# Optimization experiments

Measured on AMD Instinct MI355X. Metric: run time of the kernel, lower is better.

The kernel has to match this reference:

```python
import jax, jax.numpy as jnp
import numpy as np

FEAT_DIM = 128
GUIDE_DIM = 128
NIR_DIM = 32
H_LR, W_LR = 128, 128
H_HR, W_HR = 256, 256
IMNET_IN = FEAT_DIM + 2 * GUIDE_DIM + 2  # 386


def make_coord_1d(n):
    # pixel-center coords in [-1, 1]: (2i+1)/n - 1
    return (2.0 * jnp.arange(n, dtype=jnp.float32) + 1.0) / n - 1.0


def nearest_sample(img, cy, cx):
    """F.grid_sample(img, grid, mode='nearest', align_corners=False, padding='zeros').
    img: [b, C, h, w]; cy, cx: [N] normalized coords (cy -> h axis, cx -> w axis).
    Returns sampled values [b, C, N] and the pixel-center coords (qcy, qcx) the
    nearest sample corresponds to (0 when out of range, matching zero padding)."""
    h, w = img.shape[-2], img.shape[-1]
    iy = jnp.round(((cy + 1.0) * h - 1.0) * 0.5).astype(jnp.int32)  # round-half-even == nearbyint
    ix = jnp.round(((cx + 1.0) * w - 1.0) * 0.5).astype(jnp.int32)
    valid = (iy >= 0) & (iy < h) & (ix >= 0) & (ix < w)
    iyc = jnp.clip(iy, 0, h - 1)
    ixc = jnp.clip(ix, 0, w - 1)
    out = img[:, :, iyc, ixc]                       # [b, C, N] gather
    out = jnp.where(valid[None, None, :], out, 0.0)
    qcy = jnp.where(valid, (2.0 * iyc.astype(jnp.float32) + 1.0) / h - 1.0, 0.0)
    qcx = jnp.where(valid, (2.0 * ixc.astype(jnp.float32) + 1.0) / w - 1.0, 0.0)
    return out, qcy, qcx


def mlp(x, W1, b1, W2, b2, W3, b3):
    x = jax.nn.relu(x @ W1 + b1)
    x = jax.nn.relu(x @ W2 + b2)
    return x @ W3 + b3


def setup_inputs() -> dict:
    key = jax.random.key(0)
    ks = jax.random.split(key, 9)
    return {
        "feat": jax.random.normal(ks[0], (1, FEAT_DIM, H_LR, W_LR), jnp.float32),
        "lr_guide": jax.random.normal(ks[1], (1, GUIDE_DIM, H_LR, W_LR), jnp.float32),
        "hr_guide": jax.random.normal(ks[2], (1, GUIDE_DIM, H_HR, W_HR), jnp.float32),
        "W1": jax.random.normal(ks[3], (IMNET_IN, 256), jnp.float32) * 0.05,
        "b1": jax.random.normal(ks[4], (256,), jnp.float32) * 0.05,
        "W2": jax.random.normal(ks[5], (256, 128), jnp.float32) * 0.05,
        "b2": jax.random.normal(ks[6], (128,), jnp.float32) * 0.05,
        "W3": jax.random.normal(ks[7], (128, NIR_DIM), jnp.float32) * 0.05,
        "b3": jax.random.normal(ks[8], (NIR_DIM,), jnp.float32) * 0.05,
    }


def reference(feat, lr_guide, hr_guide, W1, b1, W2, b2, W3, b3):
    b, _, h, w = feat.shape
    _, cg, H, W = hr_guide.shape
    N = H * W
    featc = jnp.concatenate([lr_guide, feat], axis=1)        # [b, guide+feat, h, w]

    gy, gx = jnp.meshgrid(make_coord_1d(H), make_coord_1d(W), indexing="ij")
    cy = gy.reshape(-1)                                      # [N] coord[:, 0] (h axis)
    cx = gx.reshape(-1)                                      # [N] coord[:, 1] (w axis)

    q_guide_hr = hr_guide.reshape(b, cg, N).transpose(0, 2, 1)  # [b, N, cg]

    # feat_ : gather at the unshifted coord (identical across neighbors)
    feat_b, _, _ = nearest_sample(featc, cy, cx)
    feat_b = feat_b.transpose(0, 2, 1)                       # [b, N, C]

    rx = 1.0 / h
    ry = 1.0 / w
    preds, gcs = [], []
    for vx in (-1.0, 1.0):
        for vy in (-1.0, 1.0):
            q_feat, qcy, qcx = nearest_sample(featc, cy + vx * rx, cx + vy * ry)
            q_feat = q_feat.transpose(0, 2, 1)               # [b, N, C]
            rel = jnp.stack([(cy - qcy) * h, (cx - qcx) * w], axis=-1)  # [N, 2]
            rel = jnp.broadcast_to(rel[None], (b, N, 2))
            inp = jnp.concatenate([q_feat, q_guide_hr, rel], axis=-1)  # [b, N, 386]
            preds.append(mlp(inp, W1, b1, W2, b2, W3, b3))   # [b, N, NIR]
            # bilateral color weight: dot over channels [-4:-1]
            gcs.append(jnp.sum(feat_b[..., -4:-1] * q_feat[..., -4:-1], axis=-1))
    preds = jnp.stack(preds, axis=-1)                        # [b, N, NIR, 4]
    weight = jax.nn.softmax(jnp.stack(gcs, axis=-1), axis=-1)  # [b, N, 4]
    ret = jnp.sum(preds * weight[:, :, None, :], axis=-1)    # [b, N, NIR]
    return ret.transpose(0, 2, 1).reshape(b, -1, H, W)
```

## Files before the change

kernel.cpp:

```cpp
#include <hip/hip_runtime.h>
#include <hip/hip_bf16.h>


using bf16x8 = __attribute__((ext_vector_type(8))) __bf16;
using f32x4  = __attribute__((ext_vector_type(4))) float;

__device__ __forceinline__ float bf2f(unsigned short u){
  unsigned int x = ((unsigned int)u) << 16;
  return __builtin_bit_cast(float, x);
}
__device__ __forceinline__ unsigned short f2bf(float f){
  unsigned int x = __builtin_bit_cast(unsigned int, f);
  unsigned int r = x + 0x7fffu + ((x >> 16) & 1u);
  return (unsigned short)(r >> 16);
}
__device__ __forceinline__ unsigned int cvt_pk_bf16(float lo, float hi){
  unsigned int r;
  asm("v_cvt_pk_bf16_f32 %0, %1, %2" : "=v"(r) : "v"(lo), "v"(hi));
  return r;
}
__device__ __forceinline__ bf16x8 ld8(const ushort* p){
  uint4 r = *(const uint4*)p;
  return __builtin_bit_cast(bf16x8, r);
}

__device__ __forceinline__ int swzA(int row, int col){
  int p = ((row << 1) + (row >> 2)) & 7;
  return row*256 + (col ^ (p << 3));
}
__device__ __forceinline__ int swzB(int row, int col){
  int p = ((row << 1) + (row >> 2)) & 7;
  return row*128 + (col ^ (p << 3));
}
__device__ __forceinline__ int swzT(int row, int c){
  return row*256 + ((c & ~0x38) | ((((c>>3) + (c>>6) + row) & 7) << 3));
}

struct RowMeta { int spos; float relY, relX; };
__device__ __forceinline__ RowMeta row_meta(int Y, int X, int br){
  int ivx = br >> 1, ivy = br & 1;
  int validY, iy; float relY;
  if (ivx == 0){ validY = (Y >= 1);   iy = (Y-1) >> 1; relY = (Y & 1) ?  0.5f :  1.5f; }
  else         { validY = (Y <= 254); iy = (Y+1) >> 1; relY = (Y & 1) ? -1.5f : -0.5f; }
  int validX, ix; float relX;
  if (ivy == 0){ validX = (X >= 1);   ix = (X-1) >> 1; relX = (X & 1) ?  0.5f :  1.5f; }
  else         { validX = (X <= 254); ix = (X+1) >> 1; relX = (X & 1) ? -1.5f : -0.5f; }
  RowMeta r;
  if (validY && validX){ r.spos = iy*128 + ix; r.relY = relY; r.relX = relX; }
  else { r.spos = -1; r.relY = (float)Y + 0.5f - 128.0f; r.relX = (float)X + 0.5f - 128.0f; }
  return r;
}

__global__ __launch_bounds__(256) void prep(
    const float* __restrict__ W1, const float* __restrict__ W2,
    const float* __restrict__ W3,
    const float* __restrict__ lr_guide, const float* __restrict__ feat,
    ushort* __restrict__ W1t,
    ushort* __restrict__ W2t,
    ushort* __restrict__ W3t,
    ushort* __restrict__ Ft)
{
  __shared__ ushort T[32*256];
  const int b = blockIdx.x, t = threadIdx.x;
  if (b < 512){
    const int pos0 = b*32;
    #pragma unroll
    for (int i=0;i<32;i++){
      int k = i*8 + (t>>5), pos = t & 31;
      const float* src = (k < 128) ? lr_guide : feat;
      T[swzT(pos, k)] = f2bf(src[(size_t)(k & 127)*16384 + pos0 + pos]);
    }
    __syncthreads();
    const int pos = t>>3, ul = t&7;
    #pragma unroll
    for (int jj=0;jj<4;jj++){
      int c = ul*32 + jj*8;
      union { uint4 v; ushort s[8]; } x;
      x.v = *(const uint4*)&T[swzT(pos, c)];
      *(uint4*)&Ft[(size_t)(pos0+pos)*256 + c] = x.v;
    }
  } else {
    int i = (b-512)*256 + t;
    { int k = i >> 8, n = i & 255; W1t[n*384 + k] = f2bf(W1[i]); }
    if (i < 32768){ int k = i >> 7, n = i & 127; W2t[n*256 + k] = f2bf(W2[i]); }
    if (i < 4096) { int k = i >> 5, n = i & 31;  W3t[n*128 + k] = f2bf(W3[i]); }
  }
}

__global__ __launch_bounds__(256) void u_gemm(
    const ushort* __restrict__ Ft, const ushort* __restrict__ W1t,
    ushort* __restrict__ U)
{
  const int t = threadIdx.x;
  const int w = t >> 6, lane = t & 63, quad = lane >> 4, l15 = lane & 15;
  const int pos0 = (blockIdx.x >> 1) * 32;
  const int nh   = blockIdx.x & 1;

  bf16x8 af0[8], af1[8];
  #pragma unroll
  for (int kt=0; kt<8; kt++){
    const int ko = kt*32 + quad*8;
    af0[kt] = ld8(&Ft[(size_t)(pos0 +      l15)*256 + ko]);
    af1[kt] = ld8(&Ft[(size_t)(pos0 + 16 + l15)*256 + ko]);
  }
  f32x4 acc[2][2];
  #pragma unroll
  for (int a=0;a<2;a++){ acc[a][0] = f32x4{0.f,0.f,0.f,0.f}; acc[a][1] = f32x4{0.f,0.f,0.f,0.f}; }

  #pragma unroll
  for (int kt=0; kt<8; kt++){
    const int ko = kt*32 + quad*8;
    bf16x8 b0 = ld8(&W1t[(size_t)(nh*128 + w*32 +      l15)*384 + ko]);
    bf16x8 b1 = ld8(&W1t[(size_t)(nh*128 + w*32 + 16 + l15)*384 + ko]);
    acc[0][0] = __builtin_amdgcn_mfma_f32_16x16x32_bf16(af0[kt], b0, acc[0][0], 0,0,0);
    acc[0][1] = __builtin_amdgcn_mfma_f32_16x16x32_bf16(af0[kt], b1, acc[0][1], 0,0,0);
    acc[1][0] = __builtin_amdgcn_mfma_f32_16x16x32_bf16(af1[kt], b0, acc[1][0], 0,0,0);
    acc[1][1] = __builtin_amdgcn_mfma_f32_16x16x32_bf16(af1[kt], b1, acc[1][1], 0,0,0);
  }
  #pragma unroll
  for (int mt=0; mt<2; mt++)
    #pragma unroll
    for (int nt=0; nt<2; nt++){
      int n = nh*128 + w*32 + nt*16 + l15;
      #pragma unroll
      for (int r=0; r<4; r++)
        U[(size_t)(pos0 + mt*16 + quad*4 + r)*256 + n] = f2bf(acc[mt][nt][r]);
    }
}

__global__ __launch_bounds__(256, 4) void main_fused(
    const float* __restrict__ feat,
    const float* __restrict__ hr_guide,
    const float* __restrict__ W1,
    const float* __restrict__ b1v,
    const float* __restrict__ b2v,
    const float* __restrict__ b3v,
    const ushort* __restrict__ U,
    const ushort* __restrict__ W1t,
    const ushort* __restrict__ W2t,
    const ushort* __restrict__ W3t,
    float* __restrict__ outp)
{
  __shared__ __align__(16) ushort A1[64*256];
  __shared__ __align__(16) float  w1r[2][256];
  __shared__ float gcs[64];
  __shared__ float wgt[64];

  const int t = threadIdx.x;
  const int w = t >> 6, lane = t & 63, quad = lane >> 4, l15 = lane & 15;
  const int Y  = blockIdx.x >> 4;
  const int X0 = (blockIdx.x & 15) << 4;

  const int m   = t >> 2;
  const int cg  = t & 3;
  const int pix = m >> 2, br = m & 3;
  RowMeta rm = row_meta(Y, X0 + pix, br);

  uint4 uu[8];
  if (rm.spos >= 0){
    const ushort* Up = U + (size_t)rm.spos*256 + cg*8;
    #pragma unroll
    for (int jj=0; jj<8; jj++) uu[jj] = *(const uint4*)(Up + jj*32);
  } else {
    #pragma unroll
    for (int jj=0; jj<8; jj++) uu[jj] = make_uint4(0u,0u,0u,0u);
  }

  w1r[0][t] = W1[384*256 + t];
  w1r[1][t] = W1[385*256 + t];

  if (t < 64){
    RowMeta g = row_meta(Y, X0 + (t>>2), t & 3);
    float gc = 0.0f;
    if (g.spos >= 0){
      int bpos = (Y>>1)*128 + ((X0 + (t>>2)) >> 1);
      #pragma unroll
      for (int cc=0; cc<3; cc++)
        gc += feat[(size_t)(124+cc)*16384 + bpos] * feat[(size_t)(124+cc)*16384 + g.spos];
    }
    gcs[t] = gc;
  }

  {
    const float* hg = hr_guide + (size_t)Y*256 + X0 + l15;
    bf16x8 ha[4];
    #pragma unroll
    for (int kt=0; kt<4; kt++){
      float v[8];
      #pragma unroll
      for (int j=0; j<8; j++) v[j] = hg[(size_t)(kt*32 + quad*8 + j)*65536];
      uint4 pk;
      pk.x = cvt_pk_bf16(v[0],v[1]); pk.y = cvt_pk_bf16(v[2],v[3]);
      pk.z = cvt_pk_bf16(v[4],v[5]); pk.w = cvt_pk_bf16(v[6],v[7]);
      ha[kt] = __builtin_bit_cast(bf16x8, pk);
    }
    f32x4 accg[4];
    #pragma unroll
    for (int nt=0; nt<4; nt++) accg[nt] = f32x4{0.f,0.f,0.f,0.f};
    #pragma unroll
    for (int kt=0; kt<4; kt++)
      #pragma unroll
      for (int nt=0; nt<4; nt++){
        bf16x8 b = ld8(&W1t[(size_t)(w*64 + nt*16 + l15)*384 + 256 + kt*32 + quad*8]);
        accg[nt] = __builtin_amdgcn_mfma_f32_16x16x32_bf16(ha[kt], b, accg[nt], 0,0,0);
      }
    #pragma unroll
    for (int nt=0; nt<4; nt++){
      int n = w*64 + nt*16 + l15;
      float bv = b1v[n];
      #pragma unroll
      for (int r=0; r<4; r++)
        A1[swzA(32 + quad*4 + r, n)] = f2bf(accg[nt][r] + bv);
    }
  }
  __syncthreads();

  uint4 gt[8];
  #pragma unroll
  for (int jj=0; jj<8; jj++)
    gt[jj] = *(const uint4*)&A1[swzA(32 + pix, cg*8 + jj*32)];
  if (t < 16){
    float g0 = gcs[t*4+0], g1 = gcs[t*4+1], g2 = gcs[t*4+2], g3 = gcs[t*4+3];
    float mx = fmaxf(fmaxf(g0,g1), fmaxf(g2,g3));
    float e0 = __expf(g0-mx), e1 = __expf(g1-mx), e2 = __expf(g2-mx), e3 = __expf(g3-mx);
    float inv = 1.0f/(e0+e1+e2+e3);
    wgt[t*4+0]=e0*inv; wgt[t*4+1]=e1*inv; wgt[t*4+2]=e2*inv; wgt[t*4+3]=e3*inv;
  }
  __syncthreads();

  {
    const float relY = rm.relY, relX = rm.relX;
    #pragma unroll
    for (int jj=0; jj<8; jj++){
      const int c = cg*8 + jj*32;
      union { uint4 v; ushort s[8]; } gu, uv;
      gu.v = gt[jj];
      uv.v = uu[jj];
      float r0[8], r1[8];
      *(float4*)&r0[0] = *(const float4*)&w1r[0][c];
      *(float4*)&r0[4] = *(const float4*)&w1r[0][c+4];
      *(float4*)&r1[0] = *(const float4*)&w1r[1][c];
      *(float4*)&r1[4] = *(const float4*)&w1r[1][c+4];
      unsigned int ov[4];
      #pragma unroll
      for (int i=0; i<4; i++){
        float h0 = bf2f(uv.s[2*i+0]) + bf2f(gu.s[2*i+0]) + relY*r0[2*i+0] + relX*r1[2*i+0];
        float h1 = bf2f(uv.s[2*i+1]) + bf2f(gu.s[2*i+1]) + relY*r0[2*i+1] + relX*r1[2*i+1];
        ov[i] = cvt_pk_bf16(fmaxf(h0, 0.0f), fmaxf(h1, 0.0f));
      }
      *(uint4*)&A1[swzA(m, c)] = make_uint4(ov[0],ov[1],ov[2],ov[3]);
    }
  }
  __syncthreads();

  bf16x8 b2f[8][2];
  #pragma unroll
  for (int kt=0; kt<8; kt++)
    #pragma unroll
    for (int nt=0; nt<2; nt++)
      b2f[kt][nt] = ld8(&W2t[(size_t)(w*32 + nt*16 + l15)*256 + kt*32 + quad*8]);

  f32x4 acc2[4][2];
  #pragma unroll
  for (int mt=0; mt<4; mt++)
    #pragma unroll
    for (int nt=0; nt<2; nt++) acc2[mt][nt] = f32x4{0.f,0.f,0.f,0.f};

  __builtin_amdgcn_s_setprio(1);
  #pragma unroll
  for (int mt=0; mt<4; mt++)
    #pragma unroll
    for (int kt=0; kt<8; kt++){
      bf16x8 a = ld8(&A1[swzA(mt*16 + l15, kt*32 + quad*8)]);
      #pragma unroll
      for (int nt=0; nt<2; nt++)
        acc2[mt][nt] = __builtin_amdgcn_mfma_f32_16x16x32_bf16(a, b2f[kt][nt], acc2[mt][nt], 0,0,0);
    }
  __builtin_amdgcn_s_setprio(0);
  __syncthreads();

  bf16x8 b3f[4][2];
  #pragma unroll
  for (int kt=0; kt<4; kt++)
    #pragma unroll
    for (int nt=0; nt<2; nt++)
      b3f[kt][nt] = ld8(&W3t[(size_t)(nt*16 + l15)*128 + kt*32 + quad*8]);
  {
    float bias0 = b2v[w*32 + l15], bias1 = b2v[w*32 + 16 + l15];
    #pragma unroll
    for (int mt=0; mt<4; mt++)
      #pragma unroll
      for (int nt=0; nt<2; nt++){
        int n = w*32 + nt*16 + l15;
        float bv = nt ? bias1 : bias0;
        #pragma unroll
        for (int r=0; r<4; r++)
          A1[swzB(mt*16 + quad*4 + r, n)] = f2bf(fmaxf(acc2[mt][nt][r] + bv, 0.0f));
      }
  }
  __syncthreads();

  {
    f32x4 acc3[2] = { f32x4{0.f,0.f,0.f,0.f}, f32x4{0.f,0.f,0.f,0.f} };
    #pragma unroll
    for (int kt=0; kt<4; kt++){
      bf16x8 a = ld8(&A1[swzB(w*16 + l15, kt*32 + quad*8)]);
      #pragma unroll
      for (int nt=0; nt<2; nt++)
        acc3[nt] = __builtin_amdgcn_mfma_f32_16x16x32_bf16(a, b3f[kt][nt], acc3[nt], 0,0,0);
    }
    int lp = w*4 + quad;
    int X = X0 + lp;
    float w0 = wgt[lp*4+0], w1 = wgt[lp*4+1], w2 = wgt[lp*4+2], w3 = wgt[lp*4+3];
    #pragma unroll
    for (int nt=0; nt<2; nt++){
      int n = nt*16 + l15;
      float bb = b3v[n];
      float v = w0*(acc3[nt][0]+bb) + w1*(acc3[nt][1]+bb)
              + w2*(acc3[nt][2]+bb) + w3*(acc3[nt][3]+bb);
      outp[(size_t)n*65536 + (size_t)Y*256 + X] = v;
    }
  }
}

extern "C" void kernel_launch(void* const* d_in, const int* in_sizes, int n_in,
                              void* d_out, int out_size, void* d_ws, size_t ws_size,
                              hipStream_t stream)
{
  const float* feat     = (const float*)d_in[0];
  const float* lr_guide = (const float*)d_in[1];
  const float* hr_guide = (const float*)d_in[2];
  const float* W1       = (const float*)d_in[3];
  const float* b1       = (const float*)d_in[4];
  const float* W2       = (const float*)d_in[5];
  const float* b2       = (const float*)d_in[6];
  const float* W3       = (const float*)d_in[7];
  const float* b3       = (const float*)d_in[8];
  float* outp = (float*)d_out;

  char* ws = (char*)d_ws;
  ushort* W1t = (ushort*)(ws);
  ushort* W2t = (ushort*)(ws + 196608);
  ushort* W3t = (ushort*)(ws + 262144);
  ushort* Ft  = (ushort*)(ws + 270336);
  ushort* Ub  = (ushort*)(ws + 270336 + 8388608);

  prep<<<896, 256, 0, stream>>>(W1, W2, W3, lr_guide, feat, W1t, W2t, W3t, Ft);
  u_gemm<<<1024, 256, 0, stream>>>(Ft, W1t, Ub);
  main_fused<<<4096, 256, 0, stream>>>(feat, hr_guide, W1, b1, b2, b3,
                                       Ub, W1t, W2t, W3t, outp);
}
```

Baseline: 223.7 us.

## Fuse feature transpose into U GEMM and stage hr_guide via LDS

Drops the intermediate Ft buffer by having u_gemm transpose and convert lr_guide/feat tiles into shared memory itself, with each block computing all 256 output columns. In main_fused, hr_guide is loaded with coalesced float4 reads into LDS instead of strided scalar loads. The guide GEMM results go to a separate Gt buffer, W2 fragment loads are hoisted earlier, and a block-index swizzle is added. The extra LDS use and hoisted registers lower the occupancy hint from 4 to 3 blocks.

```diff
diff --git a/kernel.cpp b/kernel.cpp
--- a/kernel.cpp
+++ b/kernel.cpp
@@ -31,9 +31,6 @@
 __device__ __forceinline__ int swzB(int row, int col){
   int p = ((row << 1) + (row >> 2)) & 7;
   return row*128 + (col ^ (p << 3));
-}
-__device__ __forceinline__ int swzT(int row, int c){
-  return row*256 + ((c & ~0x38) | ((((c>>3) + (c>>6) + row) & 7) << 3));
 }
 
 struct RowMeta { int spos; float relY, relX; };
@@ -51,84 +48,70 @@
   return r;
 }
 
-__global__ __launch_bounds__(256) void prep(
+__global__ __launch_bounds__(256) void convert_weights(
     const float* __restrict__ W1, const float* __restrict__ W2,
     const float* __restrict__ W3,
-    const float* __restrict__ lr_guide, const float* __restrict__ feat,
     ushort* __restrict__ W1t,
     ushort* __restrict__ W2t,
-    ushort* __restrict__ W3t,
-    ushort* __restrict__ Ft)
+    ushort* __restrict__ W3t)
+{
+  int i = blockIdx.x*256 + threadIdx.x;
+  { int k = i >> 8, n = i & 255; W1t[n*384 + k] = f2bf(W1[i]); }
+  if (i < 32768){ int k = i >> 7, n = i & 127; W2t[n*256 + k] = f2bf(W2[i]); }
+  if (i < 4096) { int k = i >> 5, n = i & 31;  W3t[n*128 + k] = f2bf(W3[i]); }
+}
+
+__global__ __launch_bounds__(256) void u_gemm(
+    const float* __restrict__ lr_guide, const float* __restrict__ feat,
+    const ushort* __restrict__ W1t,
+    ushort* __restrict__ U)
 {
   __shared__ ushort T[32*256];
-  const int b = blockIdx.x, t = threadIdx.x;
-  if (b < 512){
-    const int pos0 = b*32;
-    #pragma unroll
-    for (int i=0;i<32;i++){
-      int k = i*8 + (t>>5), pos = t & 31;
-      const float* src = (k < 128) ? lr_guide : feat;
-      T[swzT(pos, k)] = f2bf(src[(size_t)(k & 127)*16384 + pos0 + pos]);
-    }
-    __syncthreads();
-    const int pos = t>>3, ul = t&7;
-    #pragma unroll
-    for (int jj=0;jj<4;jj++){
-      int c = ul*32 + jj*8;
-      union { uint4 v; ushort s[8]; } x;
-      x.v = *(const uint4*)&T[swzT(pos, c)];
-      *(uint4*)&Ft[(size_t)(pos0+pos)*256 + c] = x.v;
-    }
-  } else {
-    int i = (b-512)*256 + t;
-    { int k = i >> 8, n = i & 255; W1t[n*384 + k] = f2bf(W1[i]); }
-    if (i < 32768){ int k = i >> 7, n = i & 127; W2t[n*256 + k] = f2bf(W2[i]); }
-    if (i < 4096) { int k = i >> 5, n = i & 31;  W3t[n*128 + k] = f2bf(W3[i]); }
-  }
-}
-
-__global__ __launch_bounds__(256) void u_gemm(
-    const ushort* __restrict__ Ft, const ushort* __restrict__ W1t,
-    ushort* __restrict__ U)
-{
   const int t = threadIdx.x;
   const int w = t >> 6, lane = t & 63, quad = lane >> 4, l15 = lane & 15;
-  const int pos0 = (blockIdx.x >> 1) * 32;
-  const int nh   = blockIdx.x & 1;
-
-  bf16x8 af0[8], af1[8];
+  const int pos0 = blockIdx.x * 32;
+
+  #pragma unroll
+  for (int i=0; i<32; i++){
+    int k = i*8 + (t>>5), p = t & 31;
+    const float* src = (k < 128) ? lr_guide : feat;
+    T[swzA(p, k)] = f2bf(src[(size_t)(k & 127)*16384 + pos0 + p]);
+  }
+  __syncthreads();
+
+  f32x4 acc[2][4];
+  #pragma unroll
+  for (int mt=0; mt<2; mt++)
+    #pragma unroll
+    for (int nt=0; nt<4; nt++) acc[mt][nt] = f32x4{0.f,0.f,0.f,0.f};
+
   #pragma unroll
   for (int kt=0; kt<8; kt++){
     const int ko = kt*32 + quad*8;
-    af0[kt] = ld8(&Ft[(size_t)(pos0 +      l15)*256 + ko]);
-    af1[kt] = ld8(&Ft[(size_t)(pos0 + 16 + l15)*256 + ko]);
-  }
-  f32x4 acc[2][2];
-  #pragma unroll
-  for (int a=0;a<2;a++){ acc[a][0] = f32x4{0.f,0.f,0.f,0.f}; acc[a][1] = f32x4{0.f,0.f,0.f,0.f}; }
-
-  #pragma unroll
-  for (int kt=0; kt<8; kt++){
-    const int ko = kt*32 + quad*8;
-    bf16x8 b0 = ld8(&W1t[(size_t)(nh*128 + w*32 +      l15)*384 + ko]);
-    bf16x8 b1 = ld8(&W1t[(size_t)(nh*128 + w*32 + 16 + l15)*384 + ko]);
-    acc[0][0] = __builtin_amdgcn_mfma_f32_16x16x32_bf16(af0[kt], b0, acc[0][0], 0,0,0);
-    acc[0][1] = __builtin_amdgcn_mfma_f32_16x16x32_bf16(af0[kt], b1, acc[0][1], 0,0,0);
-    acc[1][0] = __builtin_amdgcn_mfma_f32_16x16x32_bf16(af1[kt], b0, acc[1][0], 0,0,0);
-    acc[1][1] = __builtin_amdgcn_mfma_f32_16x16x32_bf16(af1[kt], b1, acc[1][1], 0,0,0);
+    bf16x8 bt[4];
+    #pragma unroll
+    for (int nt=0; nt<4; nt++)
+      bt[nt] = ld8(&W1t[(size_t)(w*64 + nt*16 + l15)*384 + ko]);
+    bf16x8 a0 = ld8(&T[swzA(l15,      ko)]);
+    bf16x8 a1 = ld8(&T[swzA(16 + l15, ko)]);
+    #pragma unroll
+    for (int nt=0; nt<4; nt++){
+      acc[0][nt] = __builtin_amdgcn_mfma_f32_16x16x32_bf16(a0, bt[nt], acc[0][nt], 0,0,0);
+      acc[1][nt] = __builtin_amdgcn_mfma_f32_16x16x32_bf16(a1, bt[nt], acc[1][nt], 0,0,0);
+    }
   }
   #pragma unroll
   for (int mt=0; mt<2; mt++)
     #pragma unroll
-    for (int nt=0; nt<2; nt++){
-      int n = nh*128 + w*32 + nt*16 + l15;
+    for (int nt=0; nt<4; nt++){
+      int n = w*64 + nt*16 + l15;
       #pragma unroll
       for (int r=0; r<4; r++)
         U[(size_t)(pos0 + mt*16 + quad*4 + r)*256 + n] = f2bf(acc[mt][nt][r]);
     }
 }
 
-__global__ __launch_bounds__(256, 4) void main_fused(
+__global__ __launch_bounds__(256, 3) void main_fused(
     const float* __restrict__ feat,
     const float* __restrict__ hr_guide,
     const float* __restrict__ W1,
@@ -142,14 +125,16 @@
     float* __restrict__ outp)
 {
   __shared__ __align__(16) ushort A1[64*256];
+  __shared__ __align__(16) ushort Gt[16*256];
   __shared__ __align__(16) float  w1r[2][256];
   __shared__ float gcs[64];
   __shared__ float wgt[64];
 
   const int t = threadIdx.x;
   const int w = t >> 6, lane = t & 63, quad = lane >> 4, l15 = lane & 15;
-  const int Y  = blockIdx.x >> 4;
-  const int X0 = (blockIdx.x & 15) << 4;
+  const int wg = (blockIdx.x & 7) * 512 + (blockIdx.x >> 3);
+  const int Y  = wg >> 4;
+  const int X0 = (wg & 15) << 4;
 
   const int m   = t >> 2;
   const int cg  = t & 3;
@@ -166,6 +151,25 @@
     for (int jj=0; jj<8; jj++) uu[jj] = make_uint4(0u,0u,0u,0u);
   }
 
+  bf16x8 gb[4][4];
+  #pragma unroll
+  for (int kt=0; kt<4; kt++)
+    #pragma unroll
+    for (int nt=0; nt<4; nt++)
+      gb[kt][nt] = ld8(&W1t[(size_t)(w*64 + nt*16 + l15)*384 + 256 + kt*32 + quad*8]);
+
+  {
+    #pragma unroll
+    for (int i=0; i<2; i++){
+      int id = i*256 + t;
+      int ch = id >> 2, xq = id & 3;
+      float4 v = *(const float4*)(hr_guide + (size_t)ch*65536 + Y*256 + X0 + xq*4);
+      A1[swzB(xq*4+0, ch)] = f2bf(v.x);
+      A1[swzB(xq*4+1, ch)] = f2bf(v.y);
+      A1[swzB(xq*4+2, ch)] = f2bf(v.z);
+      A1[swzB(xq*4+3, ch)] = f2bf(v.w);
+    }
+  }
   w1r[0][t] = W1[384*256 + t];
   w1r[1][t] = W1[385*256 + t];
 
@@ -180,45 +184,8 @@
     }
     gcs[t] = gc;
   }
-
-  {
-    const float* hg = hr_guide + (size_t)Y*256 + X0 + l15;
-    bf16x8 ha[4];
-    #pragma unroll
-    for (int kt=0; kt<4; kt++){
-      float v[8];
-      #pragma unroll
-      for (int j=0; j<8; j++) v[j] = hg[(size_t)(kt*32 + quad*8 + j)*65536];
-      uint4 pk;
-      pk.x = cvt_pk_bf16(v[0],v[1]); pk.y = cvt_pk_bf16(v[2],v[3]);
-      pk.z = cvt_pk_bf16(v[4],v[5]); pk.w = cvt_pk_bf16(v[6],v[7]);
-      ha[kt] = __builtin_bit_cast(bf16x8, pk);
-    }
-    f32x4 accg[4];
-    #pragma unroll
-    for (int nt=0; nt<4; nt++) accg[nt] = f32x4{0.f,0.f,0.f,0.f};
-    #pragma unroll
-    for (int kt=0; kt<4; kt++)
-      #pragma unroll
-      for (int nt=0; nt<4; nt++){
-        bf16x8 b = ld8(&W1t[(size_t)(w*64 + nt*16 + l15)*384 + 256 + kt*32 + quad*8]);
-        accg[nt] = __builtin_amdgcn_mfma_f32_16x16x32_bf16(ha[kt], b, accg[nt], 0,0,0);
-      }
-    #pragma unroll
-    for (int nt=0; nt<4; nt++){
-      int n = w*64 + nt*16 + l15;
-      float bv = b1v[n];
-      #pragma unroll
-      for (int r=0; r<4; r++)
-        A1[swzA(32 + quad*4 + r, n)] = f2bf(accg[nt][r] + bv);
-    }
-  }
-  __syncthreads();
-
-  uint4 gt[8];
-  #pragma unroll
-  for (int jj=0; jj<8; jj++)
-    gt[jj] = *(const uint4*)&A1[swzA(32 + pix, cg*8 + jj*32)];
+  __syncthreads();
+
   if (t < 16){
     float g0 = gcs[t*4+0], g1 = gcs[t*4+1], g2 = gcs[t*4+2], g3 = gcs[t*4+3];
     float mx = fmaxf(fmaxf(g0,g1), fmaxf(g2,g3));
@@ -226,7 +193,34 @@
     float inv = 1.0f/(e0+e1+e2+e3);
     wgt[t*4+0]=e0*inv; wgt[t*4+1]=e1*inv; wgt[t*4+2]=e2*inv; wgt[t*4+3]=e3*inv;
   }
-  __syncthreads();
+  {
+    f32x4 accg[4];
+    #pragma unroll
+    for (int nt=0; nt<4; nt++) accg[nt] = f32x4{0.f,0.f,0.f,0.f};
+    #pragma unroll
+    for (int kt=0; kt<4; kt++){
+      bf16x8 a = ld8(&A1[swzB(l15, kt*32 + quad*8)]);
+      #pragma unroll
+      for (int nt=0; nt<4; nt++)
+        accg[nt] = __builtin_amdgcn_mfma_f32_16x16x32_bf16(a, gb[kt][nt], accg[nt], 0,0,0);
+    }
+    #pragma unroll
+    for (int nt=0; nt<4; nt++){
+      int n = w*64 + nt*16 + l15;
+      float bv = b1v[n];
+      #pragma unroll
+      for (int r=0; r<4; r++)
+        Gt[swzA(quad*4+r, n)] = f2bf(accg[nt][r] + bv);
+    }
+  }
+  __syncthreads();
+
+  bf16x8 b2f[8][2];
+  #pragma unroll
+  for (int kt=0; kt<8; kt++)
+    #pragma unroll
+    for (int nt=0; nt<2; nt++)
+      b2f[kt][nt] = ld8(&W2t[(size_t)(w*32 + nt*16 + l15)*256 + kt*32 + quad*8]);
 
   {
     const float relY = rm.relY, relX = rm.relX;
@@ -234,7 +228,7 @@
     for (int jj=0; jj<8; jj++){
       const int c = cg*8 + jj*32;
       union { uint4 v; ushort s[8]; } gu, uv;
-      gu.v = gt[jj];
+      gu.v = *(const uint4*)&Gt[swzA(pix, c)];
       uv.v = uu[jj];
       float r0[8], r1[8];
       *(float4*)&r0[0] = *(const float4*)&w1r[0][c];
@@ -252,13 +246,6 @@
     }
   }
   __syncthreads();
-
-  bf16x8 b2f[8][2];
-  #pragma unroll
-  for (int kt=0; kt<8; kt++)
-    #pragma unroll
-    for (int nt=0; nt<2; nt++)
-      b2f[kt][nt] = ld8(&W2t[(size_t)(w*32 + nt*16 + l15)*256 + kt*32 + quad*8]);
 
   f32x4 acc2[4][2];
   #pragma unroll
@@ -342,11 +329,10 @@
   ushort* W1t = (ushort*)(ws);
   ushort* W2t = (ushort*)(ws + 196608);
   ushort* W3t = (ushort*)(ws + 262144);
-  ushort* Ft  = (ushort*)(ws + 270336);
-  ushort* Ub  = (ushort*)(ws + 270336 + 8388608);
-
-  prep<<<896, 256, 0, stream>>>(W1, W2, W3, lr_guide, feat, W1t, W2t, W3t, Ft);
-  u_gemm<<<1024, 256, 0, stream>>>(Ft, W1t, Ub);
+  ushort* Ub  = (ushort*)(ws + 270336);
+
+  convert_weights<<<384, 256, 0, stream>>>(W1, W2, W3, W1t, W2t, W3t);
+  u_gemm<<<512, 256, 0, stream>>>(lr_guide, feat, W1t, Ub);
   main_fused<<<4096, 256, 0, stream>>>(feat, hr_guide, W1, b1, b2, b3,
                                        Ub, W1t, W2t, W3t, outp);
 }
```

Measured after the change: 190.3 us, median of 2. 1.18x faster.
